# Performance work log

Hardware: AMD Instinct MI355X
Metric: run time of the kernel (lower is better)

## Reference

```python
import jax, jax.numpy as jnp
import numpy as np

B, L, D, Y = 8, 2500, 512, 8921


def setup_inputs() -> dict:
    key = jax.random.key(0)
    k1, k2, k3, k4, k5, k6 = jax.random.split(key, 6)
    x = jax.random.normal(k1, (B, L, D), dtype=jnp.float32)
    target = jax.random.uniform(k2, (B, Y), dtype=jnp.float32)
    text_inputs = jax.random.randint(k3, (B, L), 0, 50000, dtype=jnp.int32)
    # Xavier-uniform-like init for the two [Y, D] weights
    lim = float(np.sqrt(6.0 / (Y + D)))
    U_weight = jax.random.uniform(k4, (Y, D), dtype=jnp.float32, minval=-lim, maxval=lim)
    final_weight = jax.random.uniform(k5, (Y, D), dtype=jnp.float32, minval=-lim, maxval=lim)
    final_bias = jax.random.uniform(k6, (Y,), dtype=jnp.float32, minval=-0.05, maxval=0.05)
    return {"x": x, "target": target, "text_inputs": text_inputs,
            "U_weight": U_weight, "final_weight": final_weight, "final_bias": final_bias}


def reference(x, target, text_inputs, U_weight, final_weight, final_bias):
    # att: [B, Y, L] = U.weight @ x^T
    att = jnp.einsum('yd,bld->byl', U_weight, x)
    # softmax over sequence dim
    alpha = jax.nn.softmax(att, axis=2)
    # per-label context: [B, Y, D]
    m = jnp.einsum('byl,bld->byd', alpha, x)
    # gated reduction instead of a linear layer: [B, Y]
    y = jnp.einsum('byd,yd->by', m, final_weight) + final_bias
    # BCEWithLogitsLoss (mean over all elements), numerically stable
    loss = jnp.mean(jnp.maximum(y, 0.0) - y * target + jnp.log1p(jnp.exp(-jnp.abs(y))))
    return (y, loss)
```

## Files before the change

kernel.cpp:

```cpp
#include <hip/hip_runtime.h>
#include <stdint.h>

#define B_ 8
#define L_ 2500
#define D_ 512
#define Y_ 8921
#define LP 2560
#define YP 8960
#define BLK 128
#define BK 32
#define NKT 16
#define NS 4
#define LTS 5
#define TOT (LTS * NKT)

typedef float f32x4 __attribute__((ext_vector_type(4)));
typedef __bf16 bf16x8 __attribute__((ext_vector_type(8)));
typedef unsigned short u16;
typedef unsigned int u32;

__device__ __forceinline__ u32 pack2(float a, float b) {
  u32 ua = __float_as_uint(a); ua = (ua + 0x7FFFu + ((ua >> 16) & 1u)) >> 16;
  u32 ub = __float_as_uint(b); ub = (ub + 0x7FFFu + ((ub >> 16) & 1u)) >> 16;
  return ua | (ub << 16);
}

__global__ void cvt_x_kernel(const float* __restrict__ x, u16* __restrict__ xb) {
  int idx = blockIdx.x * 256 + threadIdx.x;
  int row = idx >> 6;
  int c8  = (idx & 63) << 3;
  int b = row / LP;
  int l = row - b * LP;
  uint4 o;
  if (l < L_) {
    const float* s = x + (size_t)(b * L_ + l) * D_ + c8;
    float4 f0 = *(const float4*)s;
    float4 f1 = *(const float4*)(s + 4);
    o.x = pack2(f0.x, f0.y); o.y = pack2(f0.z, f0.w);
    o.z = pack2(f1.x, f1.y); o.w = pack2(f1.z, f1.w);
  } else {
    o = make_uint4(0u, 0u, 0u, 0u);
  }
  *(uint4*)(xb + (size_t)row * D_ + c8) = o;
}

__global__ void cvt_w_kernel(const float* __restrict__ U, const float* __restrict__ Wf,
                             u16* __restrict__ Ub, u16* __restrict__ Wb) {
  int idx = blockIdx.x * 256 + threadIdx.x;
  const int half = YP * 64;
  const float* src = U; u16* dst = Ub;
  int i = idx;
  if (idx >= half) { i -= half; src = Wf; dst = Wb; }
  int row = i >> 6;
  int c8  = (i & 63) << 3;
  uint4 o;
  if (row < Y_) {
    const float* s = src + (size_t)row * D_ + c8;
    float4 f0 = *(const float4*)s;
    float4 f1 = *(const float4*)(s + 4);
    o.x = pack2(f0.x, f0.y); o.y = pack2(f0.z, f0.w);
    o.z = pack2(f1.x, f1.y); o.w = pack2(f1.z, f1.w);
  } else {
    o = make_uint4(0u, 0u, 0u, 0u);
  }
  *(uint4*)(dst + (size_t)row * D_ + c8) = o;
}

__device__ __forceinline__ void async16(const u16* g, u16* l) {
  __builtin_amdgcn_global_load_lds(
      (const __attribute__((address_space(1))) u32*)g,
      (__attribute__((address_space(3))) u32*)l, 16, 0, 0);
}

__global__ __launch_bounds__(256, 2) void fused_kernel(
    const u16* __restrict__ xb,
    const u16* __restrict__ Ub,
    const u16* __restrict__ Wb,
    float* __restrict__ part)
{
  __shared__ __align__(16) u16 sU[2][BLK * BK];
  __shared__ __align__(16) u16 sW[2][BLK * BK];
  __shared__ __align__(16) u16 sX[2][BLK * BK];

  const int t    = threadIdx.x;
  const int lane = t & 63;
  const int wv   = t >> 6;
  const int l16  = lane & 15;
  const int q    = lane >> 4;
  const int b    = blockIdx.y;
  const int y0   = blockIdx.x * BLK;
  const int s    = blockIdx.z;

  const int srow = t >> 2;
  const int scol = (t & 3) << 3;
  const u16* gU0 = Ub + (size_t)(y0 + srow) * D_ + scol;
  const u16* gU1 = gU0 + (size_t)64 * D_;
  const u16* gW0 = Wb + (size_t)(y0 + srow) * D_ + scol;
  const u16* gW1 = gW0 + (size_t)64 * D_;
  const u16* gXb = xb + (size_t)b * LP * D_ + (size_t)srow * D_ + scol;

  float M[8], Z[8], W[8];
#pragma unroll
  for (int i = 0; i < 8; ++i) { M[i] = -1e30f; Z[i] = 0.f; W[i] = 0.f; }

  const f32x4 z4 = {0.f, 0.f, 0.f, 0.f};

  auto stage = [&](int stp, int bf) {
    const int kt = stp & (NKT - 1);
    const int lt = stp >> 4;
    const int ko = kt * BK;
    const u16* gX = gXb + (size_t)((s * LTS + lt) * BLK) * D_ + ko;
    async16(gU0 + ko, &sU[bf][t * 8]);
    async16(gU1 + ko, &sU[bf][2048 + t * 8]);
    async16(gW0 + ko, &sW[bf][t * 8]);
    async16(gW1 + ko, &sW[bf][2048 + t * 8]);
    async16(gX,                  &sX[bf][t * 8]);
    async16(gX + (size_t)64 * D_, &sX[bf][2048 + t * 8]);
  };

  stage(0, 0);

  int step = 0;
  for (int ltl = 0; ltl < LTS; ++ltl) {
    f32x4 accA[2][8], accS[2][8];
#pragma unroll
    for (int ry = 0; ry < 2; ++ry)
#pragma unroll
      for (int cl = 0; cl < 8; ++cl) { accA[ry][cl] = z4; accS[ry][cl] = z4; }

    for (int kt = 0; kt < NKT; ++kt, ++step) {
      const int nstep = step + 1;
      if (nstep < TOT) stage(nstep, nstep & 1);

      if (nstep < TOT) asm volatile("s_waitcnt vmcnt(6)" ::: "memory");
      else             asm volatile("s_waitcnt vmcnt(0)" ::: "memory");
      __builtin_amdgcn_s_barrier();
      asm volatile("" ::: "memory");

      const int cb = step & 1;
      const u16* bU = sU[cb];
      const u16* bW = sW[cb];
      const u16* bX = sX[cb];

      bf16x8 aU0 = *(const bf16x8*)(const void*)(bU + (wv * 32 + l16) * BK + q * 8);
      bf16x8 aU1 = *(const bf16x8*)(const void*)(bU + (wv * 32 + 16 + l16) * BK + q * 8);
      bf16x8 aW0 = *(const bf16x8*)(const void*)(bW + (wv * 32 + l16) * BK + q * 8);
      bf16x8 aW1 = *(const bf16x8*)(const void*)(bW + (wv * 32 + 16 + l16) * BK + q * 8);
      __builtin_amdgcn_s_setprio(1);
#pragma unroll
      for (int cl = 0; cl < 8; ++cl) {
        bf16x8 bXf = *(const bf16x8*)(const void*)(bX + (cl * 16 + l16) * BK + q * 8);
        accA[0][cl] = __builtin_amdgcn_mfma_f32_16x16x32_bf16(aU0, bXf, accA[0][cl], 0, 0, 0);
        accA[1][cl] = __builtin_amdgcn_mfma_f32_16x16x32_bf16(aU1, bXf, accA[1][cl], 0, 0, 0);
        accS[0][cl] = __builtin_amdgcn_mfma_f32_16x16x32_bf16(aW0, bXf, accS[0][cl], 0, 0, 0);
        accS[1][cl] = __builtin_amdgcn_mfma_f32_16x16x32_bf16(aW1, bXf, accS[1][cl], 0, 0, 0);
      }
      __builtin_amdgcn_s_setprio(0);
      asm volatile("" ::: "memory");
      __builtin_amdgcn_s_barrier();
    }

    const int l0 = (s * LTS + ltl) * BLK;
    const bool boundary = (l0 + BLK > L_);
#pragma unroll
    for (int ry = 0; ry < 2; ++ry) {
#pragma unroll
      for (int r = 0; r < 4; ++r) {
        const int si = ry * 4 + r;
        float a[8];
        if (boundary) {
#pragma unroll
          for (int cl = 0; cl < 8; ++cl) {
            float v = accA[ry][cl][r];
            a[cl] = (l0 + cl * 16 + l16 >= L_) ? -1e30f : v;
          }
        } else {
#pragma unroll
          for (int cl = 0; cl < 8; ++cl) a[cl] = accA[ry][cl][r];
        }
        float tmax = a[0];
#pragma unroll
        for (int cl = 1; cl < 8; ++cl) tmax = fmaxf(tmax, a[cl]);
        const float mnew  = fmaxf(M[si], tmax);
        const float scale = __expf(M[si] - mnew);
        float zl = 0.f, wl = 0.f;
#pragma unroll
        for (int cl = 0; cl < 8; ++cl) {
          float p = __expf(a[cl] - mnew);
          zl += p;
          wl = fmaf(p, accS[ry][cl][r], wl);
        }
        Z[si] = fmaf(Z[si], scale, zl);
        W[si] = fmaf(W[si], scale, wl);
        M[si] = mnew;
      }
    }
  }

#pragma unroll
  for (int si = 0; si < 8; ++si) {
    float M0 = M[si], Z0 = Z[si], W0 = W[si];
#pragma unroll
    for (int st = 1; st <= 8; st <<= 1) {
      const float Mo = __shfl_xor(M0, st);
      const float Zo = __shfl_xor(Z0, st);
      const float Wo = __shfl_xor(W0, st);
      const float mn = fmaxf(M0, Mo);
      const float sa = __expf(M0 - mn);
      const float sb = __expf(Mo - mn);
      Z0 = Z0 * sa + Zo * sb;
      W0 = W0 * sa + Wo * sb;
      M0 = mn;
    }
    M[si] = M0; Z[si] = Z0; W[si] = W0;
  }

  if (l16 == 0) {
    float* p = part + ((size_t)(b * 70 + blockIdx.x) * NS + s) * 384;
#pragma unroll
    for (int ry = 0; ry < 2; ++ry) {
#pragma unroll
      for (int r = 0; r < 4; ++r) {
        const int si = ry * 4 + r;
        const int yl = wv * 32 + ry * 16 + q * 4 + r;
        p[yl]       = M[si];
        p[128 + yl] = Z[si];
        p[256 + yl] = W[si];
      }
    }
  }
}

__global__ void combine_kernel(const float* __restrict__ part,
                               const float* __restrict__ bias,
                               const float* __restrict__ target,
                               float* __restrict__ out) {
  const int idx = blockIdx.x * 256 + threadIdx.x;
  float lpart = 0.f;
  if (idx < B_ * Y_) {
    const int b = idx / Y_;
    const int y = idx - b * Y_;
    const int yt = y >> 7, yl = y & 127;
    const float* p = part + ((size_t)(b * 70 + yt) * NS) * 384 + yl;
    float M = -1e30f;
#pragma unroll
    for (int s2 = 0; s2 < NS; ++s2) M = fmaxf(M, p[s2 * 384]);
    float Z = 0.f, W = 0.f;
#pragma unroll
    for (int s2 = 0; s2 < NS; ++s2) {
      const float e = __expf(p[s2 * 384] - M);
      Z = fmaf(p[s2 * 384 + 128], e, Z);
      W = fmaf(p[s2 * 384 + 256], e, W);
    }
    const float yv = W / Z + bias[y];
    out[idx] = yv;
    const float tg = target[idx];
    lpart = fmaxf(yv, 0.f) - yv * tg + log1pf(__expf(-fabsf(yv)));
  }
  lpart += __shfl_xor(lpart, 1);  lpart += __shfl_xor(lpart, 2);
  lpart += __shfl_xor(lpart, 4);  lpart += __shfl_xor(lpart, 8);
  lpart += __shfl_xor(lpart, 16); lpart += __shfl_xor(lpart, 32);
  if ((threadIdx.x & 63) == 0)
    atomicAdd(out + (size_t)B_ * Y_, lpart * (1.0f / (B_ * Y_)));
}

extern "C" void kernel_launch(void* const* d_in, const int* in_sizes, int n_in,
                              void* d_out, int out_size, void* d_ws, size_t ws_size,
                              hipStream_t stream) {
  const float* x      = (const float*)d_in[0];
  const float* target = (const float*)d_in[1];
  const float* U      = (const float*)d_in[3];
  const float* Wf     = (const float*)d_in[4];
  const float* bias   = (const float*)d_in[5];
  float* out = (float*)d_out;

  u16* xb = (u16*)d_ws;
  u16* Ub = xb + (size_t)B_ * LP * D_;
  u16* Wb = Ub + (size_t)YP * D_;
  float* part = (float*)(Wb + (size_t)YP * D_);

  hipMemsetAsync(out + (size_t)B_ * Y_, 0, sizeof(float), stream);
  cvt_x_kernel<<<dim3((B_ * LP * 64) / 256), 256, 0, stream>>>(x, xb);
  cvt_w_kernel<<<dim3((2 * YP * 64) / 256), 256, 0, stream>>>(U, Wf, Ub, Wb);
  fused_kernel<<<dim3(YP / BLK, B_, NS), 256, 0, stream>>>(xb, Ub, Wb, part);
  combine_kernel<<<dim3((B_ * Y_ + 255) / 256), 256, 0, stream>>>(part, bias, target, out);
}
```

Before: 585.8 us.

## Switch to 32x32x16 MFMA tiles with XOR-swizzled LDS layout

Replaces the 16x16x32 bf16 MFMA tiling with 32x32x16 MFMAs, so each wave computes 4 column tiles of 32 rows. Softmax state becomes 16 rows per lane with a 5-step shuffle reduction. The LDS staging columns are XOR-swizzled to avoid bank conflicts on the new fragment reads. The aim is fewer LDS fragment loads per FLOP and higher MFMA efficiency. The cost is more accumulator and state registers at 2 waves/SIMD, and the swizzle and output index mapping must be exactly right.

```diff
diff --git a/kernel.cpp b/kernel.cpp
--- a/kernel.cpp
+++ b/kernel.cpp
@@ -14,7 +14,7 @@
 #define LTS 5
 #define TOT (LTS * NKT)
 
-typedef float f32x4 __attribute__((ext_vector_type(4)));
+typedef float f32x16 __attribute__((ext_vector_type(16)));
 typedef __bf16 bf16x8 __attribute__((ext_vector_type(8)));
 typedef unsigned short u16;
 typedef unsigned int u32;
@@ -85,25 +85,24 @@
   const int t    = threadIdx.x;
   const int lane = t & 63;
   const int wv   = t >> 6;
-  const int l16  = lane & 15;
-  const int q    = lane >> 4;
+  const int r5   = lane & 31;
+  const int hi   = lane >> 5;
+  const int swz  = ((hi ^ ((lane >> 1) & 3)) << 3);
   const int b    = blockIdx.y;
   const int y0   = blockIdx.x * BLK;
   const int s    = blockIdx.z;
 
   const int srow = t >> 2;
-  const int scol = (t & 3) << 3;
+  const int scol = (((t & 3) ^ ((t >> 3) & 3)) << 3);
   const u16* gU0 = Ub + (size_t)(y0 + srow) * D_ + scol;
   const u16* gU1 = gU0 + (size_t)64 * D_;
   const u16* gW0 = Wb + (size_t)(y0 + srow) * D_ + scol;
   const u16* gW1 = gW0 + (size_t)64 * D_;
   const u16* gXb = xb + (size_t)b * LP * D_ + (size_t)srow * D_ + scol;
 
-  float M[8], Z[8], W[8];
-#pragma unroll
-  for (int i = 0; i < 8; ++i) { M[i] = -1e30f; Z[i] = 0.f; W[i] = 0.f; }
-
-  const f32x4 z4 = {0.f, 0.f, 0.f, 0.f};
+  float M[16], Z[16], W[16];
+#pragma unroll
+  for (int i = 0; i < 16; ++i) { M[i] = -1e30f; Z[i] = 0.f; W[i] = 0.f; }
 
   auto stage = [&](int stp, int bf) {
     const int kt = stp & (NKT - 1);
@@ -114,19 +113,21 @@
     async16(gU1 + ko, &sU[bf][2048 + t * 8]);
     async16(gW0 + ko, &sW[bf][t * 8]);
     async16(gW1 + ko, &sW[bf][2048 + t * 8]);
-    async16(gX,                  &sX[bf][t * 8]);
+    async16(gX,                   &sX[bf][t * 8]);
     async16(gX + (size_t)64 * D_, &sX[bf][2048 + t * 8]);
   };
 
   stage(0, 0);
 
+  const int rowA = wv * 32 + r5;
+
   int step = 0;
   for (int ltl = 0; ltl < LTS; ++ltl) {
-    f32x4 accA[2][8], accS[2][8];
-#pragma unroll
-    for (int ry = 0; ry < 2; ++ry)
-#pragma unroll
-      for (int cl = 0; cl < 8; ++cl) { accA[ry][cl] = z4; accS[ry][cl] = z4; }
+    f32x16 accA[4], accS[4];
+#pragma unroll
+    for (int tt = 0; tt < 4; ++tt)
+#pragma unroll
+      for (int i = 0; i < 16; ++i) { accA[tt][i] = 0.f; accS[tt][i] = 0.f; }
 
     for (int kt = 0; kt < NKT; ++kt, ++step) {
       const int nstep = step + 1;
@@ -142,18 +143,20 @@
       const u16* bW = sW[cb];
       const u16* bX = sX[cb];
 
-      bf16x8 aU0 = *(const bf16x8*)(const void*)(bU + (wv * 32 + l16) * BK + q * 8);
-      bf16x8 aU1 = *(const bf16x8*)(const void*)(bU + (wv * 32 + 16 + l16) * BK + q * 8);
-      bf16x8 aW0 = *(const bf16x8*)(const void*)(bW + (wv * 32 + l16) * BK + q * 8);
-      bf16x8 aW1 = *(const bf16x8*)(const void*)(bW + (wv * 32 + 16 + l16) * BK + q * 8);
+      bf16x8 aU0 = *(const bf16x8*)(const void*)(bU + rowA * BK + swz);
+      bf16x8 aU1 = *(const bf16x8*)(const void*)(bU + rowA * BK + (swz ^ 16));
+      bf16x8 aW0 = *(const bf16x8*)(const void*)(bW + rowA * BK + swz);
+      bf16x8 aW1 = *(const bf16x8*)(const void*)(bW + rowA * BK + (swz ^ 16));
       __builtin_amdgcn_s_setprio(1);
 #pragma unroll
-      for (int cl = 0; cl < 8; ++cl) {
-        bf16x8 bXf = *(const bf16x8*)(const void*)(bX + (cl * 16 + l16) * BK + q * 8);
-        accA[0][cl] = __builtin_amdgcn_mfma_f32_16x16x32_bf16(aU0, bXf, accA[0][cl], 0, 0, 0);
-        accA[1][cl] = __builtin_amdgcn_mfma_f32_16x16x32_bf16(aU1, bXf, accA[1][cl], 0, 0, 0);
-        accS[0][cl] = __builtin_amdgcn_mfma_f32_16x16x32_bf16(aW0, bXf, accS[0][cl], 0, 0, 0);
-        accS[1][cl] = __builtin_amdgcn_mfma_f32_16x16x32_bf16(aW1, bXf, accS[1][cl], 0, 0, 0);
+      for (int tt = 0; tt < 4; ++tt) {
+        const int rowB = tt * 32 + r5;
+        bf16x8 x0 = *(const bf16x8*)(const void*)(bX + rowB * BK + swz);
+        bf16x8 x1 = *(const bf16x8*)(const void*)(bX + rowB * BK + (swz ^ 16));
+        accA[tt] = __builtin_amdgcn_mfma_f32_32x32x16_bf16(aU0, x0, accA[tt], 0, 0, 0);
+        accA[tt] = __builtin_amdgcn_mfma_f32_32x32x16_bf16(aU1, x1, accA[tt], 0, 0, 0);
+        accS[tt] = __builtin_amdgcn_mfma_f32_32x32x16_bf16(aW0, x0, accS[tt], 0, 0, 0);
+        accS[tt] = __builtin_amdgcn_mfma_f32_32x32x16_bf16(aW1, x1, accS[tt], 0, 0, 0);
       }
       __builtin_amdgcn_s_setprio(0);
       asm volatile("" ::: "memory");
@@ -162,46 +165,41 @@
 
     const int l0 = (s * LTS + ltl) * BLK;
     const bool boundary = (l0 + BLK > L_);
-#pragma unroll
-    for (int ry = 0; ry < 2; ++ry) {
-#pragma unroll
-      for (int r = 0; r < 4; ++r) {
-        const int si = ry * 4 + r;
-        float a[8];
-        if (boundary) {
-#pragma unroll
-          for (int cl = 0; cl < 8; ++cl) {
-            float v = accA[ry][cl][r];
-            a[cl] = (l0 + cl * 16 + l16 >= L_) ? -1e30f : v;
-          }
-        } else {
-#pragma unroll
-          for (int cl = 0; cl < 8; ++cl) a[cl] = accA[ry][cl][r];
+    const int lcol = l0 + r5;
+#pragma unroll
+    for (int si = 0; si < 16; ++si) {
+      float a[4];
+      if (boundary) {
+#pragma unroll
+        for (int tt = 0; tt < 4; ++tt) {
+          float v = accA[tt][si];
+          a[tt] = (lcol + tt * 32 >= L_) ? -1e30f : v;
         }
-        float tmax = a[0];
-#pragma unroll
-        for (int cl = 1; cl < 8; ++cl) tmax = fmaxf(tmax, a[cl]);
-        const float mnew  = fmaxf(M[si], tmax);
-        const float scale = __expf(M[si] - mnew);
-        float zl = 0.f, wl = 0.f;
-#pragma unroll
-        for (int cl = 0; cl < 8; ++cl) {
-          float p = __expf(a[cl] - mnew);
-          zl += p;
-          wl = fmaf(p, accS[ry][cl][r], wl);
-        }
-        Z[si] = fmaf(Z[si], scale, zl);
-        W[si] = fmaf(W[si], scale, wl);
-        M[si] = mnew;
+      } else {
+#pragma unroll
+        for (int tt = 0; tt < 4; ++tt) a[tt] = accA[tt][si];
       }
-    }
-  }
-
-#pragma unroll
-  for (int si = 0; si < 8; ++si) {
+      const float tmax  = fmaxf(fmaxf(a[0], a[1]), fmaxf(a[2], a[3]));
+      const float mnew  = fmaxf(M[si], tmax);
+      const float scale = __expf(M[si] - mnew);
+      float zl = 0.f, wl = 0.f;
+#pragma unroll
+      for (int tt = 0; tt < 4; ++tt) {
+        float p = __expf(a[tt] - mnew);
+        zl += p;
+        wl = fmaf(p, accS[tt][si], wl);
+      }
+      Z[si] = fmaf(Z[si], scale, zl);
+      W[si] = fmaf(W[si], scale, wl);
+      M[si] = mnew;
+    }
+  }
+
+#pragma unroll
+  for (int si = 0; si < 16; ++si) {
     float M0 = M[si], Z0 = Z[si], W0 = W[si];
 #pragma unroll
-    for (int st = 1; st <= 8; st <<= 1) {
+    for (int st = 1; st <= 16; st <<= 1) {
       const float Mo = __shfl_xor(M0, st);
       const float Zo = __shfl_xor(Z0, st);
       const float Wo = __shfl_xor(W0, st);
@@ -215,18 +213,14 @@
     M[si] = M0; Z[si] = Z0; W[si] = W0;
   }
 
-  if (l16 == 0) {
+  if (r5 == 0) {
     float* p = part + ((size_t)(b * 70 + blockIdx.x) * NS + s) * 384;
 #pragma unroll
-    for (int ry = 0; ry < 2; ++ry) {
-#pragma unroll
-      for (int r = 0; r < 4; ++r) {
-        const int si = ry * 4 + r;
-        const int yl = wv * 32 + ry * 16 + q * 4 + r;
-        p[yl]       = M[si];
-        p[128 + yl] = Z[si];
-        p[256 + yl] = W[si];
-      }
+    for (int si = 0; si < 16; ++si) {
+      const int yl = wv * 32 + (si & 3) + ((si >> 2) << 3) + (hi << 2);
+      p[yl]       = M[si];
+      p[128 + yl] = Z[si];
+      p[256 + yl] = W[si];
     }
   }
 }
```

After: 629.0 us. +7.4%, slower.
